# Kernel optimization log

Measured on AMD Instinct MI355X. Metric: run time of the kernel, lower is better.

## Reference

```python
import jax, jax.numpy as jnp
import numpy as np

B_, K_, C_, HID_, T_, H_, W_ = 4, 4096, 384, 1536, 8, 32, 32
L_ = T_ * H_ * W_


def setup_inputs() -> dict:
    key = jax.random.key(0)
    ks = jax.random.split(key, 8)
    x_sparse = jax.random.normal(ks[0], (B_, K_, C_), dtype=jnp.float32)
    # unique, sorted per-batch active-token indices in [0, L)
    perm_keys = jax.random.split(ks[1], B_)
    indices = jax.vmap(lambda k: jnp.sort(jax.random.permutation(k, L_)[:K_]))(perm_keys).astype(jnp.int32)
    std = 0.02
    w1 = jax.random.normal(ks[2], (HID_, C_), dtype=jnp.float32) * std
    b1 = jnp.zeros((HID_,), dtype=jnp.float32)
    dw_w = jax.random.normal(ks[3], (HID_, 1, 3, 3), dtype=jnp.float32) * std  # depthwise OIHW, I=1
    dw_b = jnp.zeros((HID_,), dtype=jnp.float32)
    w2 = jax.random.normal(ks[4], (C_, HID_), dtype=jnp.float32) * std
    b2 = jnp.zeros((C_,), dtype=jnp.float32)
    return {"x_sparse": x_sparse, "indices": indices, "B": B_, "L": L_, "H": H_, "W": W_,
            "w1": w1, "b1": b1, "dw_w": dw_w, "dw_b": dw_b, "w2": w2, "b2": b2}


def reference(x_sparse, indices, B, L, H, W, w1, b1, dw_w, dw_b, w2, b2):
    K = x_sparse.shape[1]
    HID = w1.shape[0]
    T = L // (H * W)
    # sparse fc1: [B,K,C] @ [C,HID]
    h = jnp.einsum('bkc,hc->bkh', x_sparse, w1) + b1
    # scatter active tokens into zero-initialized dense grid [B,L,HID]
    bidx = jnp.arange(B)[:, None]  # [B,1]
    dense = jnp.zeros((B, L, HID), dtype=h.dtype).at[bidx, indices].set(h)
    # dense depthwise 3x3 conv on [B*T, HID, H, W]
    xs = dense.reshape(B * T, H, W, HID).transpose(0, 3, 1, 2)
    xs = jax.lax.conv_general_dilated(
        xs, dw_w, window_strides=(1, 1), padding='SAME',
        feature_group_count=HID,
        dimension_numbers=('NCHW', 'OIHW', 'NCHW')) + dw_b[None, :, None, None]
    flat = xs.transpose(0, 2, 3, 1).reshape(B, L, HID)
    # gather back the active tokens
    g = flat[bidx, indices]  # [B,K,HID]
    g = jax.nn.gelu(g, approximate=False)  # torch nn.GELU default is exact erf
    # sparse fc2: [B,K,HID] @ [HID,C_out]
    out = jnp.einsum('bkh,ch->bkc', g, w2) + b2
    return out
```

## Files before the change

### kernel.cpp

```cpp
#include <hip/hip_runtime.h>
#include <stdint.h>

using u16 = unsigned short;
using u32 = unsigned int;
using f32x4 = __attribute__((ext_vector_type(4))) float;
using s16x8 = __attribute__((ext_vector_type(8))) short;

#define DEVINL __device__ __forceinline__

constexpr int B_ = 4, K_ = 4096, C_ = 384, HID_ = 1536, H_ = 32, W_ = 32, L_ = 8192;
constexpr int M_ = B_ * K_;

DEVINL u16 f2bf(float f) {
    u32 u = __builtin_bit_cast(u32, f);
    u32 r = (u + 0x7FFFu + ((u >> 16) & 1u)) >> 16;
    return (u16)r;
}
DEVINL float bf2f(u16 h) {
    u32 u = ((u32)h) << 16;
    return __builtin_bit_cast(float, u);
}

__global__ __launch_bounds__(256) void convert_x_kernel(const float* __restrict__ x,
                                                        u16* __restrict__ out) {
    const int i = blockIdx.x * 256 + threadIdx.x;
    const float4* p = (const float4*)(x + (size_t)i * 8);
    float4 a = p[0], b = p[1];
    s16x8 o;
    o[0] = (short)f2bf(a.x); o[1] = (short)f2bf(a.y);
    o[2] = (short)f2bf(a.z); o[3] = (short)f2bf(a.w);
    o[4] = (short)f2bf(b.x); o[5] = (short)f2bf(b.y);
    o[6] = (short)f2bf(b.z); o[7] = (short)f2bf(b.w);
    *(s16x8*)(out + (size_t)i * 8) = o;
}

__global__ __launch_bounds__(256) void prep_small_kernel(
    const float* __restrict__ w1, const float* __restrict__ w2,
    const float* __restrict__ dww, const int* __restrict__ indices,
    u16* __restrict__ w1b, u16* __restrict__ w2b,
    float* __restrict__ dwT, int* __restrict__ pos2k) {
    const int i = blockIdx.x * 256 + threadIdx.x;
    if (i < 147456) {
        const float* src = (i < 73728) ? (w1 + (size_t)i * 8) : (w2 + (size_t)(i - 73728) * 8);
        u16* dst = (i < 73728) ? (w1b + (size_t)i * 8) : (w2b + (size_t)(i - 73728) * 8);
        float4 a = ((const float4*)src)[0];
        float4 b = ((const float4*)src)[1];
        s16x8 o;
        o[0] = (short)f2bf(a.x); o[1] = (short)f2bf(a.y);
        o[2] = (short)f2bf(a.z); o[3] = (short)f2bf(a.w);
        o[4] = (short)f2bf(b.x); o[5] = (short)f2bf(b.y);
        o[6] = (short)f2bf(b.z); o[7] = (short)f2bf(b.w);
        *(s16x8*)dst = o;
    } else if (i < 161280) {
        int t = i - 147456;
        int j = t / 1536;
        int hh = t - j * 1536;
        dwT[j * 1536 + hh] = dww[hh * 9 + j];
    } else {
        int t = i - 161280;
        int b = t >> 12;
        pos2k[(b << 13) + indices[t]] = t & 4095;
    }
}

template <bool OUT_BF16>
__global__ __launch_bounds__(256) void gemm_bt_kernel(
    const u16* __restrict__ A,
    const u16* __restrict__ Bt,
    const float* __restrict__ bias,
    void* __restrict__ Cv,
    int Mdim, int Ndim, int Kdim) {
    constexpr int BK = 32;
    __shared__ u16 As[128 * BK];
    __shared__ u16 Bs[128 * BK];

    const int tid = threadIdx.x;
    const int wave = tid >> 6;
    const int lane = tid & 63;
    const int row0 = blockIdx.x * 128;
    const int col0 = blockIdx.y * 128;

    const int sr = lane >> 2;
    const int sc = (lane & 3) * 8;

    const int wr = (wave >> 1) * 64;
    const int wc = (wave & 1) * 64;
    const int fq = lane >> 4;
    const int fr = lane & 15;

    f32x4 acc[4][4];
#pragma unroll
    for (int m = 0; m < 4; ++m)
#pragma unroll
        for (int n = 0; n < 4; ++n) acc[m][n] = f32x4{0.f, 0.f, 0.f, 0.f};

    const int ch0 = wave * 2;
    for (int k0 = 0; k0 < Kdim; k0 += BK) {
        __syncthreads();
#pragma unroll
        for (int cc = 0; cc < 2; ++cc) {
            const int ch = ch0 + cc;
            const int r = ch * 16 + sr;
            const u16* gA = A + (size_t)(row0 + r) * Kdim + k0 + sc;
            __builtin_amdgcn_global_load_lds(
                (const __attribute__((address_space(1))) void*)gA,
                (__attribute__((address_space(3))) void*)(As + ch * 512), 16, 0, 0);
            const u16* gB = Bt + (size_t)(col0 + r) * Kdim + k0 + sc;
            __builtin_amdgcn_global_load_lds(
                (const __attribute__((address_space(1))) void*)gB,
                (__attribute__((address_space(3))) void*)(Bs + ch * 512), 16, 0, 0);
        }
        __syncthreads();

        s16x8 af[4], bf_[4];
#pragma unroll
        for (int m = 0; m < 4; ++m)
            af[m] = *(const s16x8*)(As + (wr + m * 16 + fr) * 32 + fq * 8);
#pragma unroll
        for (int n = 0; n < 4; ++n)
            bf_[n] = *(const s16x8*)(Bs + (wc + n * 16 + fr) * 32 + fq * 8);
#pragma unroll
        for (int m = 0; m < 4; ++m)
#pragma unroll
            for (int n = 0; n < 4; ++n)
                acc[m][n] = __builtin_amdgcn_mfma_f32_16x16x32_bf16(af[m], bf_[n], acc[m][n], 0, 0, 0);
    }

#pragma unroll
    for (int n = 0; n < 4; ++n) {
        const int col = col0 + wc + n * 16 + fr;
        const float bv = bias[col];
#pragma unroll
        for (int m = 0; m < 4; ++m) {
            const int rowb = row0 + wr + m * 16 + fq * 4;
#pragma unroll
            for (int j = 0; j < 4; ++j) {
                float v = acc[m][n][j] + bv;
                if constexpr (OUT_BF16)
                    ((u16*)Cv)[(size_t)(rowb + j) * Ndim + col] = f2bf(v);
                else
                    ((float*)Cv)[(size_t)(rowb + j) * Ndim + col] = v;
            }
        }
    }
}

__global__ __launch_bounds__(192) void conv_gelu_kernel(
    const u16* __restrict__ h,
    const int* __restrict__ indices,
    const int* __restrict__ pos2k,
    const float* __restrict__ dwT,
    const float* __restrict__ dwb,
    u16* __restrict__ g)
{
    const int token = blockIdx.x;
    const int b = token >> 12;
    const int c0 = threadIdx.x * 8;
    const int pos = indices[token];
    const int x = pos & 31;
    const int y = (pos >> 5) & 31;
    const int tb = pos & ~1023;

    float acc[8];
    {
        float4 b0 = *(const float4*)(dwb + c0);
        float4 b1 = *(const float4*)(dwb + c0 + 4);
        acc[0] = b0.x; acc[1] = b0.y; acc[2] = b0.z; acc[3] = b0.w;
        acc[4] = b1.x; acc[5] = b1.y; acc[6] = b1.z; acc[7] = b1.w;
    }

#pragma unroll
    for (int dy = -1; dy <= 1; ++dy) {
        const int yy = y + dy;
        if (yy < 0 || yy >= 32) continue;
#pragma unroll
        for (int dx = -1; dx <= 1; ++dx) {
            const int xx = x + dx;
            if (xx < 0 || xx >= 32) continue;
            const int np = tb + (yy << 5) + xx;
            const int kp = pos2k[(b << 13) + np];
            if (kp < 0) continue;
            const int j = (dy + 1) * 3 + (dx + 1);
            const s16x8 hv = *(const s16x8*)(h + ((size_t)(b << 12) + kp) * 1536 + c0);
            const float* wp = dwT + j * 1536 + c0;
            const float4 w0 = *(const float4*)wp;
            const float4 w1v = *(const float4*)(wp + 4);
            acc[0] += bf2f((u16)hv[0]) * w0.x;
            acc[1] += bf2f((u16)hv[1]) * w0.y;
            acc[2] += bf2f((u16)hv[2]) * w0.z;
            acc[3] += bf2f((u16)hv[3]) * w0.w;
            acc[4] += bf2f((u16)hv[4]) * w1v.x;
            acc[5] += bf2f((u16)hv[5]) * w1v.y;
            acc[6] += bf2f((u16)hv[6]) * w1v.z;
            acc[7] += bf2f((u16)hv[7]) * w1v.w;
        }
    }

    s16x8 o;
#pragma unroll
    for (int q = 0; q < 8; ++q) {
        const float v = acc[q];
        const float gl = 0.5f * v * (1.0f + erff(v * 0.70710678118654752440f));
        o[q] = (short)f2bf(gl);
    }
    *(s16x8*)(g + (size_t)token * 1536 + c0) = o;
}

extern "C" void kernel_launch(void* const* d_in, const int* in_sizes, int n_in,
                              void* d_out, int out_size, void* d_ws, size_t ws_size,
                              hipStream_t stream) {
    (void)in_sizes; (void)n_in; (void)out_size; (void)ws_size;
    const float* x   = (const float*)d_in[0];
    const int* indices = (const int*)d_in[1];
    const float* w1  = (const float*)d_in[6];
    const float* b1  = (const float*)d_in[7];
    const float* dww = (const float*)d_in[8];
    const float* dwb = (const float*)d_in[9];
    const float* w2  = (const float*)d_in[10];
    const float* b2  = (const float*)d_in[11];

    char* ws = (char*)d_ws;
    size_t off = 0;
    auto alloc = [&](size_t bytes) -> void* {
        void* p = ws + off;
        off += (bytes + 255) & ~(size_t)255;
        return p;
    };
    u16*   Abf   = (u16*)alloc((size_t)M_ * C_ * 2);
    u16*   W1b   = (u16*)alloc((size_t)HID_ * C_ * 2);
    u16*   W2b   = (u16*)alloc((size_t)C_ * HID_ * 2);
    float* dwT   = (float*)alloc((size_t)9 * HID_ * 4);
    int*   pos2k = (int*)alloc((size_t)B_ * L_ * 4);
    u16*   hbuf  = (u16*)alloc((size_t)M_ * HID_ * 2);
    u16*   gbuf  = (u16*)alloc((size_t)M_ * HID_ * 2);

    hipMemsetAsync(pos2k, 0xFF, (size_t)B_ * L_ * 4, stream);
    convert_x_kernel<<<3072, 256, 0, stream>>>(x, Abf);
    prep_small_kernel<<<694, 256, 0, stream>>>(w1, w2, dww, indices, W1b, W2b, dwT, pos2k);

    dim3 g1(M_ / 128, HID_ / 128);
    gemm_bt_kernel<true><<<g1, 256, 0, stream>>>(Abf, W1b, b1, hbuf, M_, HID_, C_);

    conv_gelu_kernel<<<M_, 192, 0, stream>>>(hbuf, indices, pos2k, dwT, dwb, gbuf);

    dim3 g2(M_ / 128, C_ / 128);
    gemm_bt_kernel<false><<<g2, 256, 0, stream>>>(gbuf, W2b, b2, (float*)d_out, M_, C_, HID_);
}
```

Baseline: 216.1 us.

## Remap GEMM and conv blocks across XCDs and batch conv tokens per block

Both GEMMs now run on a flattened 1D grid, and block IDs are remapped so that consecutive logical tiles land on the same XCD (flat&7 interleave). This is meant to improve L2 locality of shared A/B tiles on the chiplet-based MI355X. The conv+GELU kernel now handles 8 tokens per block and keeps the 9x8 depthwise weights in registers instead of reloading them for every tap. That raises register pressure, with launch bounds set to 4 blocks per CU to compensate, and cuts the number of blocks by a factor of eight.

```diff
diff --git a/kernel.cpp b/kernel.cpp
--- a/kernel.cpp
+++ b/kernel.cpp
@@ -63,7 +63,7 @@
     }
 }
 
-template <bool OUT_BF16>
+template <bool OUT_BF16, int CB>
 __global__ __launch_bounds__(256) void gemm_bt_kernel(
     const u16* __restrict__ A,
     const u16* __restrict__ Bt,
@@ -74,11 +74,17 @@
     __shared__ u16 As[128 * BK];
     __shared__ u16 Bs[128 * BK];
 
+    const int flat = blockIdx.x;
+    const int per = gridDim.x >> 3;
+    const int lid = (flat & 7) * per + (flat >> 3);
+    const int rb = lid / CB;
+    const int cb = lid - rb * CB;
+    const int row0 = rb * 128;
+    const int col0 = cb * 128;
+
     const int tid = threadIdx.x;
     const int wave = tid >> 6;
     const int lane = tid & 63;
-    const int row0 = blockIdx.x * 128;
-    const int col0 = blockIdx.y * 128;
 
     const int sr = lane >> 2;
     const int sc = (lane & 3) * 8;
@@ -145,7 +151,8 @@
     }
 }
 
-__global__ __launch_bounds__(192) void conv_gelu_kernel(
+constexpr int TPB_CONV = 8;
+__global__ __launch_bounds__(192, 4) void conv_gelu_kernel(
     const u16* __restrict__ h,
     const int* __restrict__ indices,
     const int* __restrict__ pos2k,
@@ -153,57 +160,67 @@
     const float* __restrict__ dwb,
     u16* __restrict__ g)
 {
-    const int token = blockIdx.x;
-    const int b = token >> 12;
+    const int flat = blockIdx.x;
+    const int lb = (flat & 7) * ((M_ / TPB_CONV) >> 3) + (flat >> 3);
+    const int tok0 = lb * TPB_CONV;
     const int c0 = threadIdx.x * 8;
-    const int pos = indices[token];
-    const int x = pos & 31;
-    const int y = (pos >> 5) & 31;
-    const int tb = pos & ~1023;
-
-    float acc[8];
+
+    float wreg[9][8];
+#pragma unroll
+    for (int j = 0; j < 9; ++j) {
+        const float4 w0 = *(const float4*)(dwT + j * 1536 + c0);
+        const float4 w1v = *(const float4*)(dwT + j * 1536 + c0 + 4);
+        wreg[j][0] = w0.x; wreg[j][1] = w0.y; wreg[j][2] = w0.z; wreg[j][3] = w0.w;
+        wreg[j][4] = w1v.x; wreg[j][5] = w1v.y; wreg[j][6] = w1v.z; wreg[j][7] = w1v.w;
+    }
+    float bs[8];
     {
-        float4 b0 = *(const float4*)(dwb + c0);
-        float4 b1 = *(const float4*)(dwb + c0 + 4);
-        acc[0] = b0.x; acc[1] = b0.y; acc[2] = b0.z; acc[3] = b0.w;
-        acc[4] = b1.x; acc[5] = b1.y; acc[6] = b1.z; acc[7] = b1.w;
-    }
-
-#pragma unroll
-    for (int dy = -1; dy <= 1; ++dy) {
-        const int yy = y + dy;
-        if (yy < 0 || yy >= 32) continue;
-#pragma unroll
-        for (int dx = -1; dx <= 1; ++dx) {
-            const int xx = x + dx;
-            if (xx < 0 || xx >= 32) continue;
-            const int np = tb + (yy << 5) + xx;
-            const int kp = pos2k[(b << 13) + np];
-            if (kp < 0) continue;
-            const int j = (dy + 1) * 3 + (dx + 1);
-            const s16x8 hv = *(const s16x8*)(h + ((size_t)(b << 12) + kp) * 1536 + c0);
-            const float* wp = dwT + j * 1536 + c0;
-            const float4 w0 = *(const float4*)wp;
-            const float4 w1v = *(const float4*)(wp + 4);
-            acc[0] += bf2f((u16)hv[0]) * w0.x;
-            acc[1] += bf2f((u16)hv[1]) * w0.y;
-            acc[2] += bf2f((u16)hv[2]) * w0.z;
-            acc[3] += bf2f((u16)hv[3]) * w0.w;
-            acc[4] += bf2f((u16)hv[4]) * w1v.x;
-            acc[5] += bf2f((u16)hv[5]) * w1v.y;
-            acc[6] += bf2f((u16)hv[6]) * w1v.z;
-            acc[7] += bf2f((u16)hv[7]) * w1v.w;
-        }
-    }
-
-    s16x8 o;
-#pragma unroll
-    for (int q = 0; q < 8; ++q) {
-        const float v = acc[q];
-        const float gl = 0.5f * v * (1.0f + erff(v * 0.70710678118654752440f));
-        o[q] = (short)f2bf(gl);
-    }
-    *(s16x8*)(g + (size_t)token * 1536 + c0) = o;
+        const float4 b0 = *(const float4*)(dwb + c0);
+        const float4 b1 = *(const float4*)(dwb + c0 + 4);
+        bs[0] = b0.x; bs[1] = b0.y; bs[2] = b0.z; bs[3] = b0.w;
+        bs[4] = b1.x; bs[5] = b1.y; bs[6] = b1.z; bs[7] = b1.w;
+    }
+
+    for (int ti = 0; ti < TPB_CONV; ++ti) {
+        const int token = tok0 + ti;
+        const int b = token >> 12;
+        const int pos = indices[token];
+        const int x = pos & 31;
+        const int y = (pos >> 5) & 31;
+        const int tb = pos & ~1023;
+
+        float acc[8];
+#pragma unroll
+        for (int q = 0; q < 8; ++q) acc[q] = bs[q];
+
+#pragma unroll
+        for (int dy = -1; dy <= 1; ++dy) {
+            const int yy = y + dy;
+            if (yy < 0 || yy >= 32) continue;
+#pragma unroll
+            for (int dx = -1; dx <= 1; ++dx) {
+                const int xx = x + dx;
+                if (xx < 0 || xx >= 32) continue;
+                const int np = tb + (yy << 5) + xx;
+                const int kp = pos2k[(b << 13) + np];
+                if (kp < 0) continue;
+                const int j = (dy + 1) * 3 + (dx + 1);
+                const s16x8 hv = *(const s16x8*)(h + ((size_t)(b << 12) + kp) * 1536 + c0);
+#pragma unroll
+                for (int q = 0; q < 8; ++q)
+                    acc[q] += bf2f((u16)hv[q]) * wreg[j][q];
+            }
+        }
+
+        s16x8 o;
+#pragma unroll
+        for (int q = 0; q < 8; ++q) {
+            const float v = acc[q];
+            const float gl = 0.5f * v * (1.0f + erff(v * 0.70710678118654752440f));
+            o[q] = (short)f2bf(gl);
+        }
+        *(s16x8*)(g + (size_t)token * 1536 + c0) = o;
+    }
 }
 
 extern "C" void kernel_launch(void* const* d_in, const int* in_sizes, int n_in,
@@ -238,11 +255,11 @@
     convert_x_kernel<<<3072, 256, 0, stream>>>(x, Abf);
     prep_small_kernel<<<694, 256, 0, stream>>>(w1, w2, dww, indices, W1b, W2b, dwT, pos2k);
 
-    dim3 g1(M_ / 128, HID_ / 128);
-    gemm_bt_kernel<true><<<g1, 256, 0, stream>>>(Abf, W1b, b1, hbuf, M_, HID_, C_);
-
-    conv_gelu_kernel<<<M_, 192, 0, stream>>>(hbuf, indices, pos2k, dwT, dwb, gbuf);
-
-    dim3 g2(M_ / 128, C_ / 128);
-    gemm_bt_kernel<false><<<g2, 256, 0, stream>>>(gbuf, W2b, b2, (float*)d_out, M_, C_, HID_);
-}
+    gemm_bt_kernel<true, HID_ / 128><<<(M_ / 128) * (HID_ / 128), 256, 0, stream>>>(
+        Abf, W1b, b1, hbuf, M_, HID_, C_);
+
+    conv_gelu_kernel<<<M_ / TPB_CONV, 192, 0, stream>>>(hbuf, indices, pos2k, dwT, dwb, gbuf);
+
+    gemm_bt_kernel<false, C_ / 128><<<(M_ / 128) * (C_ / 128), 256, 0, stream>>>(
+        gbuf, W2b, b2, (float*)d_out, M_, C_, HID_);
+}
```

Result: no change. 217.7 us (+0.7%).
